# Kernel tuning notes

Hardware: AMD Instinct MI355X
Metric: run time of the kernel (lower is better)

The kernel has to match this reference:

```python
import jax, jax.numpy as jnp
import numpy as np

D_MODEL = 1024
N_HEADS = 16
THRESHOLD = 0.8


def setup_inputs() -> dict:
    key = jax.random.key(0)
    ks = jax.random.split(key, 12)
    B, L, D = 2, 2048, D_MODEL
    s = 1.0 / np.sqrt(D)
    return {
        "q_x": jax.random.normal(ks[0], (B, L, D), jnp.float32),
        "k_x": jax.random.normal(ks[1], (B, L, D), jnp.float32),
        "v_x": jax.random.normal(ks[2], (B, L, D), jnp.float32),
        "energy": jax.random.normal(ks[3], (B, L, D), jnp.float32),
        "Wq": jax.random.normal(ks[4], (D, D), jnp.float32) * s,
        "bq": jnp.zeros((D,), jnp.float32),
        "Wk": jax.random.normal(ks[5], (D, D), jnp.float32) * s,
        "bk": jnp.zeros((D,), jnp.float32),
        "Wv": jax.random.normal(ks[6], (D, D), jnp.float32) * s,
        "bv": jnp.zeros((D,), jnp.float32),
        "Wo": jax.random.normal(ks[7], (D, D), jnp.float32) * s,
        "bo": jnp.zeros((D,), jnp.float32),
    }


def reference(q_x, k_x, v_x, energy, Wq, bq, Wk, bk, Wv, bv, Wo, bo):
    B, L, D = q_x.shape
    H = N_HEADS
    Dh = D // H
    # projections -> (B, H, L, Dh)
    Q = (q_x @ Wq + bq).reshape(B, L, H, Dh).transpose(0, 2, 1, 3)
    K = (k_x @ Wk + bk).reshape(B, -1, H, Dh).transpose(0, 2, 1, 3)
    V = (v_x @ Wv + bv).reshape(B, -1, H, Dh).transpose(0, 2, 1, 3)
    sc = jnp.einsum("bhqd,bhkd->bhqk", Q, K) / jnp.sqrt(jnp.float32(Dh))
    # energy mask: (B, Lk) -> broadcast over heads/queries
    mask = jnp.mean(jnp.abs(energy), axis=-1) > THRESHOLD  # (B, Lk)
    sc = jnp.where(mask[:, None, None, :], sc, -jnp.inf)
    w = jnp.nan_to_num(jax.nn.softmax(sc, axis=-1), nan=0.0)
    o = jnp.einsum("bhqk,bhkd->bhqd", w, V).transpose(0, 2, 1, 3).reshape(B, L, D)
    return o @ Wo + bo
```

## Files before the change

### kernel.cpp

```cpp
#include <hip/hip_runtime.h>
#include <hip/hip_bf16.h>
#include <cstdint>

#define DEVI static __device__ __forceinline__

typedef __attribute__((ext_vector_type(8))) short s16x8;
typedef __attribute__((ext_vector_type(4))) float f32x4;
typedef __attribute__((ext_vector_type(2))) unsigned int u32x2;

DEVI unsigned short f2bf(float f) {
  union { float f; unsigned int u; } v; v.f = f;
  return (unsigned short)((v.u + 0x7FFFu + ((v.u >> 16) & 1u)) >> 16);
}

DEVI unsigned int pk2bf(float a, float b) {
  __hip_bfloat162 h2 = __float22bfloat162_rn(float2{a, b});
  return *(unsigned int*)&h2;
}

DEVI void g2l16(const void* g, void* l) {
  __builtin_amdgcn_global_load_lds((const __attribute__((address_space(1))) void*)g,
                                   (__attribute__((address_space(3))) void*)l, 16, 0, 0);
}

__global__ __launch_bounds__(256) void prep_kernel(const float* __restrict__ a,
                                                   const float* __restrict__ b,
                                                   const float* __restrict__ c,
                                                   const float* __restrict__ energy,
                                                   unsigned short* __restrict__ oa,
                                                   unsigned short* __restrict__ ob,
                                                   unsigned short* __restrict__ oc,
                                                   int* __restrict__ flags,
                                                   const float* __restrict__ W0,
                                                   const float* __restrict__ W1,
                                                   const float* __restrict__ W2,
                                                   const float* __restrict__ W3,
                                                   unsigned short* __restrict__ T0,
                                                   unsigned short* __restrict__ T1,
                                                   unsigned short* __restrict__ T2,
                                                   unsigned short* __restrict__ T3) {
  const int t = threadIdx.x;
  __shared__ float lds[64][65];
  if (blockIdx.y == 4) {
    const int x = blockIdx.x;
    if (x >= 1024) return;
    const int z = x >> 8, rem = x & 255;
    const float* W = z == 0 ? W0 : z == 1 ? W1 : z == 2 ? W2 : W3;
    unsigned short* WT = z == 0 ? T0 : z == 1 ? T1 : z == 2 ? T2 : T3;
    const int n0 = (rem >> 4) * 64, k0 = (rem & 15) * 64;
#pragma unroll
    for (int p = 0; p < 4; p++) {
      int r = p * 16 + (t >> 4);
      int cc = (t & 15) * 4;
      f32x4 v = *(const f32x4*)(W + (size_t)(k0 + r) * 1024 + n0 + cc);
      lds[r][cc] = v[0]; lds[r][cc + 1] = v[1]; lds[r][cc + 2] = v[2]; lds[r][cc + 3] = v[3];
    }
    __syncthreads();
    const int cc = t >> 2, gk = t & 3;
#pragma unroll
    for (int hv = 0; hv < 2; hv++) {
      s16x8 o;
#pragma unroll
      for (int j = 0; j < 8; j++) o[j] = (short)f2bf(lds[gk * 16 + hv * 8 + j][cc]);
      *(s16x8*)(WT + (size_t)(n0 + cc) * 1024 + k0 + gk * 16 + hv * 8) = o;
    }
    return;
  }
  if (blockIdx.y == 3) {
    const int row = blockIdx.x;
    f32x4 v = *(const f32x4*)(energy + (size_t)row * 1024 + t * 4);
    float s = fabsf(v[0]) + fabsf(v[1]) + fabsf(v[2]) + fabsf(v[3]);
#pragma unroll
    for (int off = 1; off < 64; off <<= 1) s += __shfl_xor(s, off);
    if ((t & 63) == 0) lds[0][t >> 6] = s;
    __syncthreads();
    if (t == 0) {
      float tot = lds[0][0] + lds[0][1] + lds[0][2] + lds[0][3];
      flags[row] = (tot * (1.0f / 1024.0f) > 0.8f) ? 1 : 0;
    }
    return;
  }
  if (blockIdx.x >= 2048) return;
  const float* in = blockIdx.y == 0 ? a : blockIdx.y == 1 ? b : c;
  unsigned short* out = blockIdx.y == 0 ? oa : blockIdx.y == 1 ? ob : oc;
  int i = (blockIdx.x * 256 + t) * 8;
  f32x4 x = *(const f32x4*)(in + i);
  f32x4 y = *(const f32x4*)(in + i + 4);
  s16x8 o;
  o[0] = (short)f2bf(x[0]); o[1] = (short)f2bf(x[1]);
  o[2] = (short)f2bf(x[2]); o[3] = (short)f2bf(x[3]);
  o[4] = (short)f2bf(y[0]); o[5] = (short)f2bf(y[1]);
  o[6] = (short)f2bf(y[2]); o[7] = (short)f2bf(y[3]);
  *(s16x8*)(out + i) = o;
}

__global__ __launch_bounds__(256) void scan_kernel(const int* __restrict__ flags,
                                                   int* __restrict__ pos,
                                                   int* __restrict__ cnt) {
  const int b = blockIdx.x, t = threadIdx.x;
  const int* f = flags + b * 2048;
  int loc[8], s = 0;
#pragma unroll
  for (int j = 0; j < 8; j++) { loc[j] = f[t * 8 + j]; s += loc[j]; }
  const int lane = t & 63, w = t >> 6;
  int ps = s;
#pragma unroll
  for (int off = 1; off < 64; off <<= 1) {
    int o = __shfl_up(ps, off);
    if (lane >= off) ps += o;
  }
  __shared__ int wsum[4];
  if (lane == 63) wsum[w] = ps;
  __syncthreads();
  int woff = 0;
  for (int i = 0; i < w; i++) woff += wsum[i];
  int excl = woff + ps - s;
  int* p = pos + b * 2048;
#pragma unroll
  for (int j = 0; j < 8; j++) { p[t * 8 + j] = loc[j] ? excl : -1; excl += loc[j]; }
  if (t == 255) cnt[b] = woff + ps;
}

__global__ __launch_bounds__(256) void proj_qkv(const unsigned short* __restrict__ xq,
                                                const unsigned short* __restrict__ xk,
                                                const unsigned short* __restrict__ xv,
                                                const unsigned short* __restrict__ WTq,
                                                const unsigned short* __restrict__ WTk,
                                                const unsigned short* __restrict__ WTv,
                                                const float* __restrict__ bq,
                                                const float* __restrict__ bk,
                                                const float* __restrict__ bv,
                                                unsigned short* __restrict__ Qb,
                                                unsigned short* __restrict__ Kc,
                                                unsigned short* __restrict__ VTc,
                                                const int* __restrict__ pos,
                                                float qsc) {
  const int z = blockIdx.z;
  const unsigned short* A  = z == 0 ? xq : z == 1 ? xk : xv;
  const unsigned short* BT = z == 0 ? WTq : z == 1 ? WTk : WTv;
  const float* bias        = z == 0 ? bq : z == 1 ? bk : bv;
  const int m0 = blockIdx.x * 128;
  const int n0 = blockIdx.y * 128;
  const int t = threadIdx.x;
  const int w = t >> 6, lane = t & 63;
  const int wr = w >> 1, wc = w & 1;
  const int lr = lane & 15, lg = lane >> 4;

  __shared__ __align__(16) unsigned short As[128 * 64];
  __shared__ __align__(16) unsigned short Bs[128 * 64];

  f32x4 acc[4][4] = {};

  const int sr = lane >> 3, sg = lane & 7;
  for (int kt = 0; kt < 1024; kt += 64) {
#pragma unroll
    for (int i = 0; i < 4; i++) {
      int r = (i * 4 + w) * 8 + sr;
      g2l16(A + (size_t)(m0 + r) * 1024 + kt + (sg ^ (r & 7)) * 8,
            (char*)As + (i * 4 + w) * 1024);
      g2l16(BT + (size_t)(n0 + r) * 1024 + kt + (sg ^ (r & 7)) * 8,
            (char*)Bs + (i * 4 + w) * 1024);
    }
    __syncthreads();
#pragma unroll
    for (int ks = 0; ks < 2; ks++) {
      s16x8 af[4], bf[4];
#pragma unroll
      for (int mi = 0; mi < 4; mi++) {
        int row = wr * 64 + mi * 16 + lr;
        af[mi] = *(const s16x8*)((const char*)As + row * 128 + (((ks * 4 + lg) ^ (row & 7)) * 16));
      }
#pragma unroll
      for (int nj = 0; nj < 4; nj++) {
        int row = wc * 64 + nj * 16 + lr;
        bf[nj] = *(const s16x8*)((const char*)Bs + row * 128 + (((ks * 4 + lg) ^ (row & 7)) * 16));
      }
#pragma unroll
      for (int mi = 0; mi < 4; mi++)
#pragma unroll
        for (int nj = 0; nj < 4; nj++)
          acc[mi][nj] = __builtin_amdgcn_mfma_f32_16x16x32_bf16(af[mi], bf[nj], acc[mi][nj], 0, 0, 0);
    }
    __syncthreads();
  }

  float bv2[4];
#pragma unroll
  for (int nj = 0; nj < 4; nj++) bv2[nj] = bias[n0 + wc * 64 + nj * 16 + lr];

#pragma unroll
  for (int mi = 0; mi < 4; mi++) {
    const int mb = m0 + wr * 64 + mi * 16 + lg * 4;
#pragma unroll
    for (int nj = 0; nj < 4; nj++) {
      const int n = n0 + wc * 64 + nj * 16 + lr;
      if (z == 0) {
#pragma unroll
        for (int rg = 0; rg < 4; rg++)
          Qb[(size_t)(mb + rg) * 1024 + n] = f2bf((acc[mi][nj][rg] + bv2[nj]) * qsc);
      } else if (z == 1) {
        const int h = n >> 6, dh = n & 63;
#pragma unroll
        for (int rg = 0; rg < 4; rg++) {
          int m = mb + rg;
          int b = m >> 11;
          int cp = pos[m];
          if (cp >= 0)
            Kc[((size_t)(b * 16 + h) * 2048 + cp) * 64 + dh] = f2bf(acc[mi][nj][rg] + bv2[nj]);
        }
      } else {
        const int h = n >> 6, dh = n & 63;
#pragma unroll
        for (int rg = 0; rg < 4; rg++) {
          int m = mb + rg;
          int b = m >> 11;
          int cp = pos[m];
          if (cp >= 0)
            VTc[((size_t)(b * 16 + h) * 64 + dh) * 2048 + cp] = f2bf(acc[mi][nj][rg] + bv2[nj]);
        }
      }
    }
  }
}

__global__ __launch_bounds__(256) void gemm_out(const unsigned short* __restrict__ A,
                                                const unsigned short* __restrict__ BT,
                                                const float* __restrict__ bias,
                                                float* __restrict__ out) {
  const int m0 = blockIdx.x * 128;
  const int n0 = blockIdx.y * 64;
  const int t = threadIdx.x;
  const int w = t >> 6, lane = t & 63;
  const int wr = w >> 1, wc = w & 1;
  const int lr = lane & 15, lg = lane >> 4;

  __shared__ __align__(16) unsigned short As[128 * 64];
  __shared__ __align__(16) unsigned short Bs[64 * 64];

  f32x4 acc[4][2] = {};

  const int sr = lane >> 3, sg = lane & 7;
  for (int kt = 0; kt < 1024; kt += 64) {
#pragma unroll
    for (int i = 0; i < 4; i++) {
      int r = (i * 4 + w) * 8 + sr;
      g2l16(A + (size_t)(m0 + r) * 1024 + kt + (sg ^ (r & 7)) * 8,
            (char*)As + (i * 4 + w) * 1024);
    }
#pragma unroll
    for (int i = 0; i < 2; i++) {
      int r = (i * 4 + w) * 8 + sr;
      g2l16(BT + (size_t)(n0 + r) * 1024 + kt + (sg ^ (r & 7)) * 8,
            (char*)Bs + (i * 4 + w) * 1024);
    }
    __syncthreads();
#pragma unroll
    for (int ks = 0; ks < 2; ks++) {
      s16x8 af[4], bf[2];
#pragma unroll
      for (int mi = 0; mi < 4; mi++) {
        int row = wr * 64 + mi * 16 + lr;
        af[mi] = *(const s16x8*)((const char*)As + row * 128 + (((ks * 4 + lg) ^ (row & 7)) * 16));
      }
#pragma unroll
      for (int nj = 0; nj < 2; nj++) {
        int row = wc * 32 + nj * 16 + lr;
        bf[nj] = *(const s16x8*)((const char*)Bs + row * 128 + (((ks * 4 + lg) ^ (row & 7)) * 16));
      }
#pragma unroll
      for (int mi = 0; mi < 4; mi++)
#pragma unroll
        for (int nj = 0; nj < 2; nj++)
          acc[mi][nj] = __builtin_amdgcn_mfma_f32_16x16x32_bf16(af[mi], bf[nj], acc[mi][nj], 0, 0, 0);
    }
    __syncthreads();
  }

  float bv2[2];
#pragma unroll
  for (int nj = 0; nj < 2; nj++) bv2[nj] = bias[n0 + wc * 32 + nj * 16 + lr];

#pragma unroll
  for (int mi = 0; mi < 4; mi++) {
    const int mb = m0 + wr * 64 + mi * 16 + lg * 4;
#pragma unroll
    for (int nj = 0; nj < 2; nj++) {
      const int n = n0 + wc * 32 + nj * 16 + lr;
#pragma unroll
      for (int rg = 0; rg < 4; rg++)
        out[(size_t)(mb + rg) * 1024 + n] = acc[mi][nj][rg] + bv2[nj];
    }
  }
}

__global__ __launch_bounds__(256) void attn_kernel(const unsigned short* __restrict__ Q,
                                                   const unsigned short* __restrict__ Kc,
                                                   const unsigned short* __restrict__ VTc,
                                                   const int* __restrict__ cnt,
                                                   unsigned short* __restrict__ O) {
  const int qb = blockIdx.x;
  const int bh = blockIdx.y;
  const int b = bh >> 4, h = bh & 15;
  const int t = threadIdx.x, w = t >> 6, lane = t & 63;
  const int lr = lane & 15, lg = lane >> 4;

  __shared__ __align__(16) unsigned short Ks[64 * 64];
  __shared__ __align__(16) unsigned short Vs[64 * 64];
  __shared__ __align__(16) unsigned short Ps[4][16 * 64];

  const size_t bh_off = (size_t)bh * 2048 * 64;
  const int q0 = qb * 64 + w * 16;
  const int cb = cnt[b];
  const int nkb = (cb + 63) >> 6;

  s16x8 qf[2];
#pragma unroll
  for (int ks = 0; ks < 2; ks++)
    qf[ks] = *(const s16x8*)(Q + ((size_t)(b * 2048 + q0 + lr)) * 1024 + h * 64 + ks * 32 + lg * 8);

  f32x4 oacc[4] = {};
  float lsum = 0.f;

  const int sr = lane >> 3, sg = lane & 7;
  for (int kb = 0; kb < nkb; kb++) {
#pragma unroll
    for (int i = 0; i < 2; i++) {
      int r = (i * 4 + w) * 8 + sr;
      g2l16(Kc + bh_off + (size_t)(kb * 64 + r) * 64 + (sg ^ (r & 7)) * 8,
            (char*)Ks + (i * 4 + w) * 1024);
    }
#pragma unroll
    for (int i = 0; i < 2; i++) {
      int r = (i * 4 + w) * 8 + sr;
      g2l16(VTc + bh_off + (size_t)r * 2048 + kb * 64 + (sg ^ (r & 7)) * 8,
            (char*)Vs + (i * 4 + w) * 1024);
    }
    __syncthreads();

    float p[4][4];
    __builtin_amdgcn_s_setprio(1);
#pragma unroll
    for (int t4 = 0; t4 < 4; t4++) {
      f32x4 s = {};
#pragma unroll
      for (int ks = 0; ks < 2; ks++) {
        int row = t4 * 16 + lr;
        s16x8 kf = *(const s16x8*)((const char*)Ks + row * 128 + (((ks * 4 + lg) ^ (row & 7)) * 16));
        s = __builtin_amdgcn_mfma_f32_16x16x32_bf16(kf, qf[ks], s, 0, 0, 0);
      }
      p[t4][0] = s[0]; p[t4][1] = s[1]; p[t4][2] = s[2]; p[t4][3] = s[3];
    }
    __builtin_amdgcn_s_setprio(0);

    if ((kb + 1) * 64 <= cb) {
#pragma unroll
      for (int t4 = 0; t4 < 4; t4++)
#pragma unroll
        for (int rg = 0; rg < 4; rg++) {
          float e = __builtin_amdgcn_exp2f(p[t4][rg]);
          p[t4][rg] = e;
          lsum += e;
        }
    } else {
      const int kbase = kb * 64 + lg * 4;
#pragma unroll
      for (int t4 = 0; t4 < 4; t4++)
#pragma unroll
        for (int rg = 0; rg < 4; rg++) {
          float e = __builtin_amdgcn_exp2f(p[t4][rg]);
          e = (kbase + t4 * 16 + rg < cb) ? e : 0.f;
          p[t4][rg] = e;
          lsum += e;
        }
    }

#pragma unroll
    for (int t4 = 0; t4 < 4; t4++) {
      u32x2 pw = {pk2bf(p[t4][0], p[t4][1]), pk2bf(p[t4][2], p[t4][3])};
      int byte = lr * 128 + ((t4 * 32 + lg * 8) ^ ((lr & 7) << 4));
      *(u32x2*)((char*)Ps + w * 2048 + byte) = pw;
    }

    __builtin_amdgcn_s_setprio(1);
#pragma unroll
    for (int ks = 0; ks < 2; ks++) {
      int byteA = lr * 128 + ((ks * 64 + lg * 16) ^ ((lr & 7) << 4));
      s16x8 af = *(const s16x8*)((const char*)Ps + w * 2048 + byteA);
#pragma unroll
      for (int dt = 0; dt < 4; dt++) {
        int row = dt * 16 + lr;
        s16x8 vf = *(const s16x8*)((const char*)Vs + row * 128 + (((ks * 4 + lg) ^ (row & 7)) * 16));
        oacc[dt] = __builtin_amdgcn_mfma_f32_16x16x32_bf16(af, vf, oacc[dt], 0, 0, 0);
      }
    }
    __builtin_amdgcn_s_setprio(0);
    __syncthreads();
  }

  lsum += __shfl_xor(lsum, 16);
  lsum += __shfl_xor(lsum, 32);

  float rinv[4];
#pragma unroll
  for (int rg = 0; rg < 4; rg++) {
    float ls = __shfl(lsum, lg * 4 + rg);
    rinv[rg] = (ls > 0.f) ? 1.0f / ls : 0.f;
  }
#pragma unroll
  for (int dt = 0; dt < 4; dt++)
#pragma unroll
    for (int rg = 0; rg < 4; rg++) {
      int q = q0 + lg * 4 + rg;
      int d = dt * 16 + lr;
      O[((size_t)(b * 2048 + q)) * 1024 + h * 64 + d] = f2bf(oacc[dt][rg] * rinv[rg]);
    }
}

extern "C" void kernel_launch(void* const* d_in, const int* in_sizes, int n_in,
                              void* d_out, int out_size, void* d_ws, size_t ws_size,
                              hipStream_t stream) {
  (void)in_sizes; (void)n_in; (void)out_size; (void)ws_size;
  const float* q_x = (const float*)d_in[0];
  const float* k_x = (const float*)d_in[1];
  const float* v_x = (const float*)d_in[2];
  const float* energy = (const float*)d_in[3];
  const float* Wq = (const float*)d_in[4];
  const float* bq = (const float*)d_in[5];
  const float* Wk = (const float*)d_in[6];
  const float* bk = (const float*)d_in[7];
  const float* Wv = (const float*)d_in[8];
  const float* bv = (const float*)d_in[9];
  const float* Wo = (const float*)d_in[10];
  const float* bo = (const float*)d_in[11];

  char* ws = (char*)d_ws;
  const size_t MB = 1024 * 1024;
  unsigned short* xq  = (unsigned short*)(ws + 0);
  unsigned short* xk  = (unsigned short*)(ws + 8 * MB);
  unsigned short* xv  = (unsigned short*)(ws + 16 * MB);
  unsigned short* WTq = (unsigned short*)(ws + 24 * MB);
  unsigned short* WTk = (unsigned short*)(ws + 26 * MB);
  unsigned short* WTv = (unsigned short*)(ws + 28 * MB);
  unsigned short* WTo = (unsigned short*)(ws + 30 * MB);
  unsigned short* Qb  = (unsigned short*)(ws + 32 * MB);
  unsigned short* Kc  = (unsigned short*)(ws + 40 * MB);
  unsigned short* VTc = (unsigned short*)(ws + 48 * MB);
  int* flags          = (int*)(ws + 56 * MB);
  int* pos            = (int*)(ws + 56 * MB + 16 * 1024);
  int* cnt            = (int*)(ws + 56 * MB + 32 * 1024);
  unsigned short* Ob  = xq;

  const float QSC = 0.18033688011112042f;

  prep_kernel<<<dim3(4096, 5), 256, 0, stream>>>(q_x, k_x, v_x, energy, xq, xk, xv, flags,
                                                 Wq, Wk, Wv, Wo, WTq, WTk, WTv, WTo);
  scan_kernel<<<2, 256, 0, stream>>>(flags, pos, cnt);

  proj_qkv<<<dim3(32, 8, 3), 256, 0, stream>>>(xq, xk, xv, WTq, WTk, WTv, bq, bk, bv,
                                               Qb, Kc, VTc, pos, QSC);

  attn_kernel<<<dim3(32, 32), 256, 0, stream>>>(Qb, Kc, VTc, cnt, Ob);

  gemm_out<<<dim3(32, 16), 256, 0, stream>>>(Ob, WTo, bo, (float*)d_out);
}
```

Baseline: 123.6 us.

## Gather only unmasked K/V rows in projection and skip fully masked tiles

```diff
diff --git a/kernel.cpp b/kernel.cpp
--- a/kernel.cpp
+++ b/kernel.cpp
@@ -39,35 +39,26 @@
                                                    unsigned short* __restrict__ T1,
                                                    unsigned short* __restrict__ T2,
                                                    unsigned short* __restrict__ T3) {
+  const int gid = blockIdx.x;
   const int t = threadIdx.x;
   __shared__ float lds[64][65];
-  if (blockIdx.y == 4) {
-    const int x = blockIdx.x;
-    if (x >= 1024) return;
-    const int z = x >> 8, rem = x & 255;
-    const float* W = z == 0 ? W0 : z == 1 ? W1 : z == 2 ? W2 : W3;
-    unsigned short* WT = z == 0 ? T0 : z == 1 ? T1 : z == 2 ? T2 : T3;
-    const int n0 = (rem >> 4) * 64, k0 = (rem & 15) * 64;
-#pragma unroll
-    for (int p = 0; p < 4; p++) {
-      int r = p * 16 + (t >> 4);
-      int cc = (t & 15) * 4;
-      f32x4 v = *(const f32x4*)(W + (size_t)(k0 + r) * 1024 + n0 + cc);
-      lds[r][cc] = v[0]; lds[r][cc + 1] = v[1]; lds[r][cc + 2] = v[2]; lds[r][cc + 3] = v[3];
-    }
-    __syncthreads();
-    const int cc = t >> 2, gk = t & 3;
-#pragma unroll
-    for (int hv = 0; hv < 2; hv++) {
-      s16x8 o;
-#pragma unroll
-      for (int j = 0; j < 8; j++) o[j] = (short)f2bf(lds[gk * 16 + hv * 8 + j][cc]);
-      *(s16x8*)(WT + (size_t)(n0 + cc) * 1024 + k0 + gk * 16 + hv * 8) = o;
-    }
+  if (gid < 6144) {
+    const float* in = gid < 2048 ? a : gid < 4096 ? b : c;
+    unsigned short* out = gid < 2048 ? oa : gid < 4096 ? ob : oc;
+    const int blk = gid & 2047;
+    int i = (blk * 256 + t) * 8;
+    f32x4 x = *(const f32x4*)(in + i);
+    f32x4 y = *(const f32x4*)(in + i + 4);
+    s16x8 o;
+    o[0] = (short)f2bf(x[0]); o[1] = (short)f2bf(x[1]);
+    o[2] = (short)f2bf(x[2]); o[3] = (short)f2bf(x[3]);
+    o[4] = (short)f2bf(y[0]); o[5] = (short)f2bf(y[1]);
+    o[6] = (short)f2bf(y[2]); o[7] = (short)f2bf(y[3]);
+    *(s16x8*)(out + i) = o;
     return;
   }
-  if (blockIdx.y == 3) {
-    const int row = blockIdx.x;
+  if (gid < 10240) {
+    const int row = gid - 6144;
     f32x4 v = *(const f32x4*)(energy + (size_t)row * 1024 + t * 4);
     float s = fabsf(v[0]) + fabsf(v[1]) + fabsf(v[2]) + fabsf(v[3]);
 #pragma unroll
@@ -80,25 +71,37 @@
     }
     return;
   }
-  if (blockIdx.x >= 2048) return;
-  const float* in = blockIdx.y == 0 ? a : blockIdx.y == 1 ? b : c;
-  unsigned short* out = blockIdx.y == 0 ? oa : blockIdx.y == 1 ? ob : oc;
-  int i = (blockIdx.x * 256 + t) * 8;
-  f32x4 x = *(const f32x4*)(in + i);
-  f32x4 y = *(const f32x4*)(in + i + 4);
-  s16x8 o;
-  o[0] = (short)f2bf(x[0]); o[1] = (short)f2bf(x[1]);
-  o[2] = (short)f2bf(x[2]); o[3] = (short)f2bf(x[3]);
-  o[4] = (short)f2bf(y[0]); o[5] = (short)f2bf(y[1]);
-  o[6] = (short)f2bf(y[2]); o[7] = (short)f2bf(y[3]);
-  *(s16x8*)(out + i) = o;
+  const int x = gid - 10240;
+  const int z = x >> 8, rem = x & 255;
+  const float* W = z == 0 ? W0 : z == 1 ? W1 : z == 2 ? W2 : W3;
+  unsigned short* WT = z == 0 ? T0 : z == 1 ? T1 : z == 2 ? T2 : T3;
+  const int n0 = (rem >> 4) * 64, k0 = (rem & 15) * 64;
+#pragma unroll
+  for (int p = 0; p < 4; p++) {
+    int r = p * 16 + (t >> 4);
+    int cc = (t & 15) * 4;
+    f32x4 v = *(const f32x4*)(W + (size_t)(k0 + r) * 1024 + n0 + cc);
+    lds[r][cc] = v[0]; lds[r][cc + 1] = v[1]; lds[r][cc + 2] = v[2]; lds[r][cc + 3] = v[3];
+  }
+  __syncthreads();
+  const int cc = t >> 2, gk = t & 3;
+#pragma unroll
+  for (int hv = 0; hv < 2; hv++) {
+    s16x8 o;
+#pragma unroll
+    for (int j = 0; j < 8; j++) o[j] = (short)f2bf(lds[gk * 16 + hv * 8 + j][cc]);
+    *(s16x8*)(WT + (size_t)(n0 + cc) * 1024 + k0 + gk * 16 + hv * 8) = o;
+  }
 }
 
 __global__ __launch_bounds__(256) void scan_kernel(const int* __restrict__ flags,
-                                                   int* __restrict__ pos,
+                                                   int* __restrict__ inv,
                                                    int* __restrict__ cnt) {
   const int b = blockIdx.x, t = threadIdx.x;
   const int* f = flags + b * 2048;
+  int* iv = inv + b * 2048;
+#pragma unroll
+  for (int j = 0; j < 8; j++) iv[t * 8 + j] = 0;
   int loc[8], s = 0;
 #pragma unroll
   for (int j = 0; j < 8; j++) { loc[j] = f[t * 8 + j]; s += loc[j]; }
@@ -115,9 +118,10 @@
   int woff = 0;
   for (int i = 0; i < w; i++) woff += wsum[i];
   int excl = woff + ps - s;
-  int* p = pos + b * 2048;
-#pragma unroll
-  for (int j = 0; j < 8; j++) { p[t * 8 + j] = loc[j] ? excl : -1; excl += loc[j]; }
+#pragma unroll
+  for (int j = 0; j < 8; j++) {
+    if (loc[j]) { iv[excl] = t * 8 + j; excl++; }
+  }
   if (t == 255) cnt[b] = woff + ps;
 }
 
@@ -133,90 +137,104 @@
                                                 unsigned short* __restrict__ Qb,
                                                 unsigned short* __restrict__ Kc,
                                                 unsigned short* __restrict__ VTc,
-                                                const int* __restrict__ pos,
+                                                const int* __restrict__ inv,
+                                                const int* __restrict__ cnt,
                                                 float qsc) {
   const int z = blockIdx.z;
+  const int m0 = blockIdx.x * 128;
+  const int n0 = blockIdx.y * 64;
+  const int b = m0 >> 11;
+  const int lc0 = m0 & 2047;
+  const int cb = (z == 0) ? 2048 : cnt[b];
+  if (lc0 >= cb) return;
+
   const unsigned short* A  = z == 0 ? xq : z == 1 ? xk : xv;
   const unsigned short* BT = z == 0 ? WTq : z == 1 ? WTk : WTv;
   const float* bias        = z == 0 ? bq : z == 1 ? bk : bv;
-  const int m0 = blockIdx.x * 128;
-  const int n0 = blockIdx.y * 128;
+
   const int t = threadIdx.x;
   const int w = t >> 6, lane = t & 63;
   const int wr = w >> 1, wc = w & 1;
   const int lr = lane & 15, lg = lane >> 4;
+  const int sr = lane >> 3, sg = lane & 7;
+
+  int srow[4];
+#pragma unroll
+  for (int i = 0; i < 4; i++) {
+    int r = (i * 4 + w) * 8 + sr;
+    srow[i] = (z == 0) ? (m0 + r) : (b * 2048 + inv[b * 2048 + lc0 + r]);
+  }
 
   __shared__ __align__(16) unsigned short As[128 * 64];
-  __shared__ __align__(16) unsigned short Bs[128 * 64];
-
-  f32x4 acc[4][4] = {};
-
-  const int sr = lane >> 3, sg = lane & 7;
+  __shared__ __align__(16) unsigned short Bs[64 * 64];
+
+  f32x4 acc[4][2] = {};
+
   for (int kt = 0; kt < 1024; kt += 64) {
 #pragma unroll
     for (int i = 0; i < 4; i++) {
       int r = (i * 4 + w) * 8 + sr;
-      g2l16(A + (size_t)(m0 + r) * 1024 + kt + (sg ^ (r & 7)) * 8,
+      g2l16(A + (size_t)srow[i] * 1024 + kt + (sg ^ (r & 7)) * 8,
             (char*)As + (i * 4 + w) * 1024);
+    }
+#pragma unroll
+    for (int i = 0; i < 2; i++) {
+      int r = (i * 4 + w) * 8 + sr;
       g2l16(BT + (size_t)(n0 + r) * 1024 + kt + (sg ^ (r & 7)) * 8,
             (char*)Bs + (i * 4 + w) * 1024);
     }
     __syncthreads();
 #pragma unroll
     for (int ks = 0; ks < 2; ks++) {
-      s16x8 af[4], bf[4];
+      s16x8 af[4], bf[2];
 #pragma unroll
       for (int mi = 0; mi < 4; mi++) {
         int row = wr * 64 + mi * 16 + lr;
         af[mi] = *(const s16x8*)((const char*)As + row * 128 + (((ks * 4 + lg) ^ (row & 7)) * 16));
       }
 #pragma unroll
-      for (int nj = 0; nj < 4; nj++) {
-        int row = wc * 64 + nj * 16 + lr;
+      for (int nj = 0; nj < 2; nj++) {
+        int row = wc * 32 + nj * 16 + lr;
         bf[nj] = *(const s16x8*)((const char*)Bs + row * 128 + (((ks * 4 + lg) ^ (row & 7)) * 16));
       }
 #pragma unroll
       for (int mi = 0; mi < 4; mi++)
 #pragma unroll
-        for (int nj = 0; nj < 4; nj++)
+        for (int nj = 0; nj < 2; nj++)
           acc[mi][nj] = __builtin_amdgcn_mfma_f32_16x16x32_bf16(af[mi], bf[nj], acc[mi][nj], 0, 0, 0);
     }
     __syncthreads();
   }
 
-  float bv2[4];
-#pragma unroll
-  for (int nj = 0; nj < 4; nj++) bv2[nj] = bias[n0 + wc * 64 + nj * 16 + lr];
+  float bv2[2];
+#pragma unroll
+  for (int nj = 0; nj < 2; nj++) bv2[nj] = bias[n0 + wc * 32 + nj * 16 + lr];
 
 #pragma unroll
   for (int mi = 0; mi < 4; mi++) {
-    const int mb = m0 + wr * 64 + mi * 16 + lg * 4;
-#pragma unroll
-    for (int nj = 0; nj < 4; nj++) {
-      const int n = n0 + wc * 64 + nj * 16 + lr;
+    const int mloc = wr * 64 + mi * 16 + lg * 4;
+#pragma unroll
+    for (int nj = 0; nj < 2; nj++) {
+      const int n = n0 + wc * 32 + nj * 16 + lr;
       if (z == 0) {
 #pragma unroll
         for (int rg = 0; rg < 4; rg++)
-          Qb[(size_t)(mb + rg) * 1024 + n] = f2bf((acc[mi][nj][rg] + bv2[nj]) * qsc);
+          Qb[(size_t)(m0 + mloc + rg) * 1024 + n] = f2bf((acc[mi][nj][rg] + bv2[nj]) * qsc);
       } else if (z == 1) {
         const int h = n >> 6, dh = n & 63;
 #pragma unroll
         for (int rg = 0; rg < 4; rg++) {
-          int m = mb + rg;
-          int b = m >> 11;
-          int cp = pos[m];
-          if (cp >= 0)
-            Kc[((size_t)(b * 16 + h) * 2048 + cp) * 64 + dh] = f2bf(acc[mi][nj][rg] + bv2[nj]);
+          int lc = lc0 + mloc + rg;
+          if (lc < cb)
+            Kc[((size_t)(b * 16 + h) * 2048 + lc) * 64 + dh] = f2bf(acc[mi][nj][rg] + bv2[nj]);
         }
       } else {
         const int h = n >> 6, dh = n & 63;
 #pragma unroll
         for (int rg = 0; rg < 4; rg++) {
-          int m = mb + rg;
-          int b = m >> 11;
-          int cp = pos[m];
-          if (cp >= 0)
-            VTc[((size_t)(b * 16 + h) * 64 + dh) * 2048 + cp] = f2bf(acc[mi][nj][rg] + bv2[nj]);
+          int lc = lc0 + mloc + rg;
+          if (lc < cb)
+            VTc[((size_t)(b * 16 + h) * 64 + dh) * 2048 + lc] = f2bf(acc[mi][nj][rg] + bv2[nj]);
         }
       }
     }
@@ -233,13 +251,13 @@
   const int w = t >> 6, lane = t & 63;
   const int wr = w >> 1, wc = w & 1;
   const int lr = lane & 15, lg = lane >> 4;
+  const int sr = lane >> 3, sg = lane & 7;
 
   __shared__ __align__(16) unsigned short As[128 * 64];
   __shared__ __align__(16) unsigned short Bs[64 * 64];
 
   f32x4 acc[4][2] = {};
 
-  const int sr = lane >> 3, sg = lane & 7;
   for (int kt = 0; kt < 1024; kt += 64) {
 #pragma unroll
     for (int i = 0; i < 4; i++) {
@@ -298,8 +316,8 @@
                                                    const unsigned short* __restrict__ VTc,
                                                    const int* __restrict__ cnt,
                                                    unsigned short* __restrict__ O) {
-  const int qb = blockIdx.x;
-  const int bh = blockIdx.y;
+  const int bh = blockIdx.x;
+  const int qb = blockIdx.y;
   const int b = bh >> 4, h = bh & 15;
   const int t = threadIdx.x, w = t >> 6, lane = t & 63;
   const int lr = lane & 15, lg = lane >> 4;
@@ -446,18 +464,18 @@
   unsigned short* Kc  = (unsigned short*)(ws + 40 * MB);
   unsigned short* VTc = (unsigned short*)(ws + 48 * MB);
   int* flags          = (int*)(ws + 56 * MB);
-  int* pos            = (int*)(ws + 56 * MB + 16 * 1024);
+  int* inv            = (int*)(ws + 56 * MB + 16 * 1024);
   int* cnt            = (int*)(ws + 56 * MB + 32 * 1024);
   unsigned short* Ob  = xq;
 
   const float QSC = 0.18033688011112042f;
 
-  prep_kernel<<<dim3(4096, 5), 256, 0, stream>>>(q_x, k_x, v_x, energy, xq, xk, xv, flags,
-                                                 Wq, Wk, Wv, Wo, WTq, WTk, WTv, WTo);
-  scan_kernel<<<2, 256, 0, stream>>>(flags, pos, cnt);
-
-  proj_qkv<<<dim3(32, 8, 3), 256, 0, stream>>>(xq, xk, xv, WTq, WTk, WTv, bq, bk, bv,
-                                               Qb, Kc, VTc, pos, QSC);
+  prep_kernel<<<11264, 256, 0, stream>>>(q_x, k_x, v_x, energy, xq, xk, xv, flags,
+                                         Wq, Wk, Wv, Wo, WTq, WTk, WTv, WTo);
+  scan_kernel<<<2, 256, 0, stream>>>(flags, inv, cnt);
+
+  proj_qkv<<<dim3(32, 16, 3), 256, 0, stream>>>(xq, xk, xv, WTq, WTk, WTv, bq, bk, bv,
+                                                Qb, Kc, VTc, inv, cnt, QSC);
 
   attn_kernel<<<dim3(32, 32), 256, 0, stream>>>(Qb, Kc, VTc, cnt, Ob);
 
```

Result: faster. 107.4 us (-13.1%).
